# Kernel optimization log

Hardware: AMD Instinct MI355X
Metric: run time of the kernel (lower is better)

Reference implementation:

```python
import jax, jax.numpy as jnp
import numpy as np

B, T, C = 2, 4096, 768
N_HEAD = 12
HEAD_DIM = C // N_HEAD


def setup_inputs() -> dict:
    key = jax.random.key(0)
    k1, k2, k3, k4, k5 = jax.random.split(key, 5)
    scale = 1.0 / np.sqrt(C)
    x = jax.random.normal(k1, (B, T, C), dtype=jnp.float32)
    # weights stored as [in, out] (transpose of torch Linear weight)
    W_attn = jax.random.normal(k2, (C, 3 * C), dtype=jnp.float32) * scale
    b_attn = jax.random.normal(k3, (3 * C,), dtype=jnp.float32) * 0.01
    W_proj = jax.random.normal(k4, (C, C), dtype=jnp.float32) * scale
    b_proj = jax.random.normal(k5, (C,), dtype=jnp.float32) * 0.01
    return {"x": x, "W_attn": W_attn, "b_attn": b_attn, "W_proj": W_proj, "b_proj": b_proj}


def reference(x, W_attn, b_attn, W_proj, b_proj):
    Bq, Tq, Cq = x.shape
    qkv = x @ W_attn + b_attn                      # [B, T, 3C]
    q, k, v = jnp.split(qkv, 3, axis=-1)           # each [B, T, C]

    def heads(t):
        return t.reshape(Bq, Tq, N_HEAD, HEAD_DIM).transpose(0, 2, 1, 3)  # [B, H, T, D]

    q, k, v = heads(q), heads(k), heads(v)
    att = jnp.einsum('bhqd,bhkd->bhqk', q, k) * (1.0 / np.sqrt(HEAD_DIM))  # [B, H, T, T]
    causal = jnp.tril(jnp.ones((Tq, Tq), dtype=bool))                      # [T, T]
    att = jnp.where(causal[None, None], att, jnp.finfo(att.dtype).min)
    att = jax.nn.softmax(att, axis=-1)
    y = jnp.einsum('bhqk,bhkd->bhqd', att, v)      # [B, H, T, D]
    y = y.transpose(0, 2, 1, 3).reshape(Bq, Tq, Cq)
    return y @ W_proj + b_proj
```

## Files before the change

### kernel.cpp

```cpp
#include <hip/hip_runtime.h>


#define TSEQ   4096
#define NHEAD  12
#define CDIM   768
#define C3     2304
#define BT_TOT 8192

#define PSTR   72

typedef __bf16 bf16x8 __attribute__((ext_vector_type(8)));
typedef __bf16 bf16x2 __attribute__((ext_vector_type(2)));
typedef float  f32x4  __attribute__((ext_vector_type(4)));

__device__ __forceinline__ unsigned short f2bf(float f) {
  unsigned int u = __builtin_bit_cast(unsigned int, f);
  u += 0x7FFFu + ((u >> 16) & 1u);
  return (unsigned short)(u >> 16);
}

__device__ __forceinline__ unsigned int pack2bf(float a, float b) {
  bf16x2 v = {(__bf16)a, (__bf16)b};
  return __builtin_bit_cast(unsigned int, v);
}

__device__ __forceinline__ f32x4 mfma16(bf16x8 a, bf16x8 b, f32x4 c) {
  return __builtin_amdgcn_mfma_f32_16x16x32_bf16(a, b, c, 0, 0, 0);
}

typedef const __attribute__((address_space(1))) void* gas_ptr;
typedef __attribute__((address_space(3))) void* las_ptr;

#define LGKM_WAIT() __builtin_amdgcn_s_waitcnt(0xC07F)


__global__ __launch_bounds__(256) void cast_f32_bf16(const float* __restrict__ x,
                                                     unsigned short* __restrict__ o, int n) {
  int i = (blockIdx.x * 256 + threadIdx.x) * 4;
  if (i < n) {
    float4 v = *(const float4*)(x + i);
    ushort4 u;
    u.x = f2bf(v.x); u.y = f2bf(v.y); u.z = f2bf(v.z); u.w = f2bf(v.w);
    *(ushort4*)(o + i) = u;
  }
}

__global__ __launch_bounds__(256) void transpose_cast(const float* __restrict__ src,
                                                      unsigned short* __restrict__ dst,
                                                      int K, int N) {
  __shared__ float tile[32][33];
  int n0 = blockIdx.x * 32, k0 = blockIdx.y * 32;
  int tx = threadIdx.x, ty = threadIdx.y;
#pragma unroll
  for (int i = 0; i < 4; ++i)
    tile[ty + i * 8][tx] = src[(size_t)(k0 + ty + i * 8) * N + n0 + tx];
  __syncthreads();
#pragma unroll
  for (int i = 0; i < 4; ++i)
    dst[(size_t)(n0 + ty + i * 8) * K + k0 + tx] = f2bf(tile[tx][ty + i * 8]);
}


__device__ __forceinline__ void gemm_bt_mainloop(const unsigned short* __restrict__ A,
                                                 const unsigned short* __restrict__ BTm,
                                                 int K, int m0, int n0,
                                                 unsigned short* lds, f32x4 acc[4][4]) {
  const int tid = threadIdx.x;
  const int wave = tid >> 6, lane = tid & 63;
  const int quad = lane >> 4, l16 = lane & 15;
  const int wm = (wave >> 1) * 64, wn = (wave & 1) * 64;
  const int srow = tid >> 2;
  const int scol = (tid & 3) * 8;

  for (int k0 = 0; k0 < K; k0 += 32) {
    __syncthreads();
#pragma unroll
    for (int r = 0; r < 2; ++r) {
      const unsigned short* ga = A + (size_t)(m0 + r * 64 + srow) * K + k0 + scol;
      __builtin_amdgcn_global_load_lds((gas_ptr)ga,
          (las_ptr)(lds + r * 2048 + wave * 512), 16, 0, 0);
      const unsigned short* gb = BTm + (size_t)(n0 + r * 64 + srow) * K + k0 + scol;
      __builtin_amdgcn_global_load_lds((gas_ptr)gb,
          (las_ptr)(lds + 4096 + r * 2048 + wave * 512), 16, 0, 0);
    }
    __syncthreads();

    bf16x8 af[4], bfr[4];
#pragma unroll
    for (int i = 0; i < 4; ++i) {
      af[i]  = *(const bf16x8*)(lds + (wm + i * 16 + l16) * 32 + quad * 8);
      bfr[i] = *(const bf16x8*)(lds + 4096 + (wn + i * 16 + l16) * 32 + quad * 8);
    }
#pragma unroll
    for (int i = 0; i < 4; ++i)
#pragma unroll
      for (int j = 0; j < 4; ++j)
        acc[i][j] = mfma16(af[i], bfr[j], acc[i][j]);
  }
}

__global__ __launch_bounds__(256) void gemm_qkv_kernel(
    const unsigned short* __restrict__ A, const unsigned short* __restrict__ BTm,
    const float* __restrict__ bias,
    unsigned short* __restrict__ qbuf, unsigned short* __restrict__ kbuf,
    unsigned short* __restrict__ vtbuf) {
  __shared__ __align__(16) unsigned short lds[128 * 136];
  f32x4 zero = {0.f, 0.f, 0.f, 0.f};
  f32x4 acc[4][4];
#pragma unroll
  for (int i = 0; i < 4; ++i)
#pragma unroll
    for (int j = 0; j < 4; ++j) acc[i][j] = zero;

  const int m0 = blockIdx.y * 128, n0 = blockIdx.x * 128;
  gemm_bt_mainloop(A, BTm, CDIM, m0, n0, lds, acc);

  const int tid = threadIdx.x;
  const int wave = tid >> 6, lane = tid & 63;
  const int quad = lane >> 4, l16 = lane & 15;
  const int wm = (wave >> 1) * 64, wn = (wave & 1) * 64;
  const float KSCALE = 0.125f * 1.44269504088896340736f;

  const int seg = n0 / CDIM;
  const float mult = (seg == 1) ? KSCALE : 1.0f;

  __syncthreads();
#pragma unroll
  for (int j = 0; j < 4; ++j) {
    const int nl = wn + j * 16 + l16;
    const float bv = bias[n0 + nl];
#pragma unroll
    for (int i = 0; i < 4; ++i) {
#pragma unroll
      for (int r = 0; r < 4; ++r) {
        const int ml = wm + i * 16 + quad * 4 + r;
        unsigned short val = f2bf((acc[i][j][r] + bv) * mult);
        if (seg < 2) lds[ml * 136 + nl] = val;
        else         lds[nl * 136 + ml] = val;
      }
    }
  }
  __syncthreads();

  const int row = tid >> 1, half = tid & 1;
  const unsigned short* src = lds + row * 136 + half * 64;
  unsigned short* dst;
  if (seg < 2) {
    const int m = m0 + row, b = m >> 12, t = m & (TSEQ - 1);
    const int nn = (n0 - seg * CDIM) + half * 64;
    const int h = nn >> 6;
    unsigned short* base = (seg == 0) ? qbuf : kbuf;
    dst = base + ((size_t)(b * NHEAD + h) * TSEQ + t) * 64;
  } else {
    const int nn = (n0 - 2 * CDIM) + row;
    const int h = nn >> 6, d = nn & 63;
    const int b = m0 >> 12, t0 = (m0 & (TSEQ - 1)) + half * 64;
    dst = vtbuf + ((size_t)(b * NHEAD + h) * 64 + d) * TSEQ + t0;
  }
#pragma unroll
  for (int k = 0; k < 8; ++k)
    *(uint4*)(dst + k * 8) = *(const uint4*)(src + k * 8);
}

__global__ __launch_bounds__(256) void gemm_out_kernel(
    const unsigned short* __restrict__ A, const unsigned short* __restrict__ BTm,
    const float* __restrict__ bias, float* __restrict__ out) {
  __shared__ __align__(16) unsigned short lds[8192];
  f32x4 zero = {0.f, 0.f, 0.f, 0.f};
  f32x4 acc[4][4];
#pragma unroll
  for (int i = 0; i < 4; ++i)
#pragma unroll
    for (int j = 0; j < 4; ++j) acc[i][j] = zero;

  const int m0 = blockIdx.y * 128, n0 = blockIdx.x * 128;
  gemm_bt_mainloop(A, BTm, CDIM, m0, n0, lds, acc);

  const int tid = threadIdx.x;
  const int wave = tid >> 6, lane = tid & 63;
  const int quad = lane >> 4, l16 = lane & 15;
  const int wm = (wave >> 1) * 64, wn = (wave & 1) * 64;

#pragma unroll
  for (int j = 0; j < 4; ++j) {
    int n = n0 + wn + j * 16 + l16;
    float bv = bias[n];
#pragma unroll
    for (int i = 0; i < 4; ++i) {
#pragma unroll
      for (int r = 0; r < 4; ++r) {
        int m = m0 + wm + i * 16 + quad * 4 + r;
        out[(size_t)m * CDIM + n] = acc[i][j][r] + bv;
      }
    }
  }
}


__device__ __forceinline__ void stage_kv(const unsigned short* __restrict__ Kp,
                                         const unsigned short* __restrict__ Vp,
                                         int j0, unsigned short* kb, unsigned short* vb,
                                         int tid, int wave) {
  const int row = tid >> 3;
  const int col = ((tid & 7) ^ (row & 7)) * 8;
  __builtin_amdgcn_global_load_lds((gas_ptr)(Kp + (size_t)(j0 + row) * 64 + col),
                                   (las_ptr)(kb + wave * 512), 16, 0, 0);
  __builtin_amdgcn_global_load_lds((gas_ptr)(Vp + (size_t)row * TSEQ + j0 + col),
                                   (las_ptr)(vb + wave * 512), 16, 0, 0);
}

__device__ __forceinline__ void qk_score(const bf16x8 kf[8], const bf16x8 qf[2], f32x4 s[4]) {
  f32x4 zero = {0.f, 0.f, 0.f, 0.f};
#pragma unroll
  for (int i = 0; i < 4; ++i)
    s[i] = mfma16(kf[2 * i + 1], qf[1], mfma16(kf[2 * i], qf[0], zero));
}

template <bool MASKED>
__device__ __forceinline__ void exp_write(const f32x4 s[4], unsigned short* __restrict__ prow,
                                          int j0, int q0, int l16, int quad, float& lsum) {
#pragma unroll
  for (int i = 0; i < 4; ++i) {
    float p[4];
#pragma unroll
    for (int r = 0; r < 4; ++r) {
      p[r] = __builtin_amdgcn_exp2f(s[i][r]);
      if (MASKED) {
        if (j0 + i * 16 + quad * 4 + r > q0 + l16) p[r] = 0.f;
      }
      lsum += p[r];
    }
    uint2 w;
    w.x = pack2bf(p[0], p[1]);
    w.y = pack2bf(p[2], p[3]);
    *(uint2*)(prow + l16 * PSTR + i * 16 + quad * 4) = w;
  }
}

__device__ __forceinline__ void pv8(const unsigned short* __restrict__ vb, int kcol0,
                                    const unsigned short* __restrict__ prow,
                                    int l16, int quad, f32x4 o[4]) {
  bf16x8 pf0 = *(const bf16x8*)(prow + l16 * PSTR + quad * 8);
  bf16x8 pf1 = *(const bf16x8*)(prow + l16 * PSTR + 32 + quad * 8);
#pragma unroll
  for (int dt = 0; dt < 4; ++dt) {
    bf16x8 v0 = *(const bf16x8*)(vb + (16 * dt + l16) * 64 + kcol0);
    bf16x8 v1 = *(const bf16x8*)(vb + (16 * dt + l16) * 64 + (kcol0 ^ 32));
    o[dt] = mfma16(pf1, v1, mfma16(pf0, v0, o[dt]));
  }
}

__global__ __launch_bounds__(512, 3) void attn_kernel(const unsigned short* __restrict__ qbuf,
                                                      const unsigned short* __restrict__ kbuf,
                                                      const unsigned short* __restrict__ vtbuf,
                                                      unsigned short* __restrict__ y) {
  __shared__ __align__(16) unsigned short k_lds[2][64 * 64];
  __shared__ __align__(16) unsigned short v_lds[2][64 * 64];
  __shared__ __align__(16) unsigned short p_lds[8][16 * PSTR];

  const int tid = threadIdx.x;
  const int wave = tid >> 6, lane = tid & 63;
  const int quad = lane >> 4, l16 = lane & 15;

  const int bh = blockIdx.x % 24;
  const int p = blockIdx.x / 24;
  const bool isA = wave < 4;
  const int qtile = isA ? p : (63 - p);
  const int q0 = qtile * 64 + (wave & 3) * 16;

  const unsigned short* Qp = qbuf + (size_t)bh * TSEQ * 64;
  const unsigned short* Kp = kbuf + (size_t)bh * TSEQ * 64;
  const unsigned short* Vp = vtbuf + (size_t)bh * 64 * TSEQ;
  unsigned short* prow = &p_lds[wave][0];

  bf16x8 qf[2];
  qf[0] = *(const bf16x8*)(Qp + (size_t)(q0 + l16) * 64 + quad * 8);
  qf[1] = *(const bf16x8*)(Qp + (size_t)(q0 + l16) * 64 + 32 + quad * 8);

  f32x4 zero = {0.f, 0.f, 0.f, 0.f};
  f32x4 o[4];
#pragma unroll
  for (int dt = 0; dt < 4; ++dt) o[dt] = zero;
  float ls = 0.f;

  const int kcol0 = (quad ^ (l16 & 7)) * 8;
  const int ntiles = 64 - p;
  const int lasttile = isA ? p : (ntiles - 1);

  stage_kv(Kp, Vp, 0, k_lds[0], v_lds[0], tid, wave);

  for (int jt = 0; jt < ntiles; ++jt) {
    __syncthreads();
    if (jt + 1 < ntiles)
      stage_kv(Kp, Vp, (jt + 1) * 64, k_lds[(jt + 1) & 1], v_lds[(jt + 1) & 1], tid, wave);

    if (jt <= lasttile) {
      const unsigned short* kb = k_lds[jt & 1];
      const unsigned short* vb = v_lds[jt & 1];
      const int j0 = jt * 64;

      bf16x8 kf[8];
#pragma unroll
      for (int i = 0; i < 4; ++i) {
        kf[2 * i]     = *(const bf16x8*)(kb + (16 * i + l16) * 64 + kcol0);
        kf[2 * i + 1] = *(const bf16x8*)(kb + (16 * i + l16) * 64 + (kcol0 ^ 32));
      }

      f32x4 s[4];
      qk_score(kf, qf, s);
      if (jt == lasttile) exp_write<true>(s, prow, j0, q0, l16, quad, ls);
      else                exp_write<false>(s, prow, j0, q0, l16, quad, ls);

      LGKM_WAIT();

      pv8(vb, kcol0, prow, l16, quad, o);
    }
  }

  ls += __shfl_xor(ls, 16); ls += __shfl_xor(ls, 32);

  const int b = bh / NHEAD, h = bh - b * NHEAD;
#pragma unroll
  for (int r = 0; r < 4; ++r) {
    const int qrow = quad * 4 + r;
    float lq = __shfl(ls, (lane & 48) + qrow);
    float inv = 1.0f / lq;
    size_t row = (size_t)(b * TSEQ + q0 + qrow) * CDIM + h * 64;
#pragma unroll
    for (int dt = 0; dt < 4; ++dt)
      y[row + dt * 16 + l16] = f2bf(o[dt][r] * inv);
  }
}


extern "C" void kernel_launch(void* const* d_in, const int* in_sizes, int n_in,
                              void* d_out, int out_size, void* d_ws, size_t ws_size,
                              hipStream_t stream) {
  const float* x      = (const float*)d_in[0];
  const float* W_attn = (const float*)d_in[1];
  const float* b_attn = (const float*)d_in[2];
  const float* W_proj = (const float*)d_in[3];
  const float* b_proj = (const float*)d_in[4];
  float* out = (float*)d_out;

  unsigned short* xb    = (unsigned short*)d_ws;
  unsigned short* WaT   = xb + (size_t)BT_TOT * CDIM;
  unsigned short* WpT   = WaT + (size_t)C3 * CDIM;
  unsigned short* qbuf  = WpT + (size_t)CDIM * CDIM;
  unsigned short* kbuf  = qbuf + (size_t)2 * NHEAD * TSEQ * 64;
  unsigned short* vtbuf = kbuf + (size_t)2 * NHEAD * TSEQ * 64;
  unsigned short* ybuf  = xb;

  cast_f32_bf16<<<(BT_TOT * CDIM) / 1024, 256, 0, stream>>>(x, xb, BT_TOT * CDIM);
  transpose_cast<<<dim3(C3 / 32, CDIM / 32), dim3(32, 8), 0, stream>>>(W_attn, WaT, CDIM, C3);
  transpose_cast<<<dim3(CDIM / 32, CDIM / 32), dim3(32, 8), 0, stream>>>(W_proj, WpT, CDIM, CDIM);

  gemm_qkv_kernel<<<dim3(C3 / 128, BT_TOT / 128), 256, 0, stream>>>(xb, WaT, b_attn,
                                                                    qbuf, kbuf, vtbuf);
  attn_kernel<<<dim3(24 * 32), 512, 0, stream>>>(qbuf, kbuf, vtbuf, ybuf);
  gemm_out_kernel<<<dim3(CDIM / 128, BT_TOT / 128), 256, 0, stream>>>(ybuf, WpT, b_proj, out);
}
```

Baseline: 234.4 us.

## Keep softmax probabilities in registers by permuting V layout for PV MFMA

The attention kernel no longer writes the exp'd scores to an LDS scratch and reads them back. Instead the score fragment is packed directly into bf16x8 MFMA operands, and the PV product is computed as V^T·P^T. To make that work, the QKV epilogue now writes V^T with a permuted key ordering, and the output store writes packed 4-element chunks per lane. Dropping p_lds frees shared memory, so launch bounds rise to 6 blocks per CU, at the cost of register pressure and a more intricate layout contract between kernels.

```diff
diff --git a/kernel.cpp b/kernel.cpp
--- a/kernel.cpp
+++ b/kernel.cpp
@@ -7,11 +7,10 @@
 #define C3     2304
 #define BT_TOT 8192
 
-#define PSTR   72
-
 typedef __bf16 bf16x8 __attribute__((ext_vector_type(8)));
 typedef __bf16 bf16x2 __attribute__((ext_vector_type(2)));
 typedef float  f32x4  __attribute__((ext_vector_type(4)));
+typedef unsigned int u32x4 __attribute__((ext_vector_type(4)));
 
 __device__ __forceinline__ unsigned short f2bf(float f) {
   unsigned int u = __builtin_bit_cast(unsigned int, f);
@@ -30,8 +29,6 @@
 
 typedef const __attribute__((address_space(1))) void* gas_ptr;
 typedef __attribute__((address_space(3))) void* las_ptr;
-
-#define LGKM_WAIT() __builtin_amdgcn_s_waitcnt(0xC07F)
 
 
 __global__ __launch_bounds__(256) void cast_f32_bf16(const float* __restrict__ x,
@@ -144,22 +141,29 @@
 
   const int row = tid >> 1, half = tid & 1;
   const unsigned short* src = lds + row * 136 + half * 64;
-  unsigned short* dst;
   if (seg < 2) {
     const int m = m0 + row, b = m >> 12, t = m & (TSEQ - 1);
     const int nn = (n0 - seg * CDIM) + half * 64;
     const int h = nn >> 6;
     unsigned short* base = (seg == 0) ? qbuf : kbuf;
-    dst = base + ((size_t)(b * NHEAD + h) * TSEQ + t) * 64;
+    unsigned short* dst = base + ((size_t)(b * NHEAD + h) * TSEQ + t) * 64;
+#pragma unroll
+    for (int k = 0; k < 8; ++k)
+      *(uint4*)(dst + k * 8) = *(const uint4*)(src + k * 8);
   } else {
     const int nn = (n0 - 2 * CDIM) + row;
     const int h = nn >> 6, d = nn & 63;
     const int b = m0 >> 12, t0 = (m0 & (TSEQ - 1)) + half * 64;
-    dst = vtbuf + ((size_t)(b * NHEAD + h) * 64 + d) * TSEQ + t0;
-  }
-#pragma unroll
-  for (int k = 0; k < 8; ++k)
-    *(uint4*)(dst + k * 8) = *(const uint4*)(src + k * 8);
+    unsigned short* dst = vtbuf + ((size_t)(b * NHEAD + h) * 64 + d) * TSEQ + t0;
+#pragma unroll
+    for (int k = 0; k < 8; ++k) {
+      const int s0 = 32 * (k >> 2) + 4 * (k & 3);
+      uint2 a = *(const uint2*)(src + s0);
+      uint2 c = *(const uint2*)(src + s0 + 16);
+      uint4 w = {a.x, a.y, c.x, c.y};
+      *(uint4*)(dst + k * 8) = w;
+    }
+  }
 }
 
 __global__ __launch_bounds__(256) void gemm_out_kernel(
@@ -217,8 +221,9 @@
 }
 
 template <bool MASKED>
-__device__ __forceinline__ void exp_write(const f32x4 s[4], unsigned short* __restrict__ prow,
-                                          int j0, int q0, int l16, int quad, float& lsum) {
+__device__ __forceinline__ void exp_pack(const f32x4 s[4], int j0, int qabs,
+                                         int l16, int quad, float& lsum, bf16x8 pf[2]) {
+  unsigned int w[8];
 #pragma unroll
   for (int i = 0; i < 4; ++i) {
     float p[4];
@@ -226,41 +231,42 @@
     for (int r = 0; r < 4; ++r) {
       p[r] = __builtin_amdgcn_exp2f(s[i][r]);
       if (MASKED) {
-        if (j0 + i * 16 + quad * 4 + r > q0 + l16) p[r] = 0.f;
+        if (j0 + i * 16 + quad * 4 + r > qabs) p[r] = 0.f;
       }
       lsum += p[r];
     }
-    uint2 w;
-    w.x = pack2bf(p[0], p[1]);
-    w.y = pack2bf(p[2], p[3]);
-    *(uint2*)(prow + l16 * PSTR + i * 16 + quad * 4) = w;
-  }
-}
-
-__device__ __forceinline__ void pv8(const unsigned short* __restrict__ vb, int kcol0,
-                                    const unsigned short* __restrict__ prow,
-                                    int l16, int quad, f32x4 o[4]) {
-  bf16x8 pf0 = *(const bf16x8*)(prow + l16 * PSTR + quad * 8);
-  bf16x8 pf1 = *(const bf16x8*)(prow + l16 * PSTR + 32 + quad * 8);
+    w[2 * i]     = pack2bf(p[0], p[1]);
+    w[2 * i + 1] = pack2bf(p[2], p[3]);
+  }
+  u32x4 lo = {w[0], w[1], w[2], w[3]};
+  u32x4 hi = {w[4], w[5], w[6], w[7]};
+  pf[0] = __builtin_bit_cast(bf16x8, lo);
+  pf[1] = __builtin_bit_cast(bf16x8, hi);
+}
+
+__device__ __forceinline__ void pv(const unsigned short* __restrict__ vb,
+                                   int l16, int quad, int x7,
+                                   const bf16x8 pf[2], f32x4 o[4]) {
 #pragma unroll
   for (int dt = 0; dt < 4; ++dt) {
-    bf16x8 v0 = *(const bf16x8*)(vb + (16 * dt + l16) * 64 + kcol0);
-    bf16x8 v1 = *(const bf16x8*)(vb + (16 * dt + l16) * 64 + (kcol0 ^ 32));
-    o[dt] = mfma16(pf1, v1, mfma16(pf0, v0, o[dt]));
-  }
-}
-
-__global__ __launch_bounds__(512, 3) void attn_kernel(const unsigned short* __restrict__ qbuf,
+    const unsigned short* vr = vb + (dt * 16 + l16) * 64;
+    bf16x8 v0 = *(const bf16x8*)(vr + ((quad ^ x7) * 8));
+    bf16x8 v1 = *(const bf16x8*)(vr + (((4 + quad) ^ x7) * 8));
+    o[dt] = mfma16(v1, pf[1], mfma16(v0, pf[0], o[dt]));
+  }
+}
+
+__global__ __launch_bounds__(512, 6) void attn_kernel(const unsigned short* __restrict__ qbuf,
                                                       const unsigned short* __restrict__ kbuf,
                                                       const unsigned short* __restrict__ vtbuf,
                                                       unsigned short* __restrict__ y) {
   __shared__ __align__(16) unsigned short k_lds[2][64 * 64];
   __shared__ __align__(16) unsigned short v_lds[2][64 * 64];
-  __shared__ __align__(16) unsigned short p_lds[8][16 * PSTR];
 
   const int tid = threadIdx.x;
   const int wave = tid >> 6, lane = tid & 63;
   const int quad = lane >> 4, l16 = lane & 15;
+  const int x7 = l16 & 7;
 
   const int bh = blockIdx.x % 24;
   const int p = blockIdx.x / 24;
@@ -271,7 +277,6 @@
   const unsigned short* Qp = qbuf + (size_t)bh * TSEQ * 64;
   const unsigned short* Kp = kbuf + (size_t)bh * TSEQ * 64;
   const unsigned short* Vp = vtbuf + (size_t)bh * 64 * TSEQ;
-  unsigned short* prow = &p_lds[wave][0];
 
   bf16x8 qf[2];
   qf[0] = *(const bf16x8*)(Qp + (size_t)(q0 + l16) * 64 + quad * 8);
@@ -283,7 +288,7 @@
   for (int dt = 0; dt < 4; ++dt) o[dt] = zero;
   float ls = 0.f;
 
-  const int kcol0 = (quad ^ (l16 & 7)) * 8;
+  const int kcol0 = (quad ^ x7) * 8;
   const int ntiles = 64 - p;
   const int lasttile = isA ? p : (ntiles - 1);
 
@@ -308,27 +313,26 @@
 
       f32x4 s[4];
       qk_score(kf, qf, s);
-      if (jt == lasttile) exp_write<true>(s, prow, j0, q0, l16, quad, ls);
-      else                exp_write<false>(s, prow, j0, q0, l16, quad, ls);
-
-      LGKM_WAIT();
-
-      pv8(vb, kcol0, prow, l16, quad, o);
+
+      bf16x8 pf[2];
+      if (jt == lasttile) exp_pack<true>(s, j0, q0 + l16, l16, quad, ls, pf);
+      else                exp_pack<false>(s, j0, q0 + l16, l16, quad, ls, pf);
+
+      pv(vb, l16, quad, x7, pf, o);
     }
   }
 
   ls += __shfl_xor(ls, 16); ls += __shfl_xor(ls, 32);
-
-  const int b = bh / NHEAD, h = bh - b * NHEAD;
-#pragma unroll
-  for (int r = 0; r < 4; ++r) {
-    const int qrow = quad * 4 + r;
-    float lq = __shfl(ls, (lane & 48) + qrow);
-    float inv = 1.0f / lq;
-    size_t row = (size_t)(b * TSEQ + q0 + qrow) * CDIM + h * 64;
-#pragma unroll
-    for (int dt = 0; dt < 4; ++dt)
-      y[row + dt * 16 + l16] = f2bf(o[dt][r] * inv);
+  const float inv = 1.0f / ls;
+
+  const int b = bh / NHEAD, hd = bh - b * NHEAD;
+  unsigned short* yr = y + (size_t)(b * TSEQ + q0 + l16) * CDIM + hd * 64 + quad * 4;
+#pragma unroll
+  for (int dt = 0; dt < 4; ++dt) {
+    uint2 w;
+    w.x = pack2bf(o[dt][0] * inv, o[dt][1] * inv);
+    w.y = pack2bf(o[dt][2] * inv, o[dt][3] * inv);
+    *(uint2*)(yr + dt * 16) = w;
   }
 }
 
```

Result: no change. 232.5 us (-0.8%).
